# Performance work log

Measured on AMD Instinct MI355X. Metric: run time of the kernel, lower is better.

Reference implementation:

```python
import jax, jax.numpy as jnp
import numpy as np

B, L, D, H, O = 128, 256, 512, 1024, 2


def setup_inputs() -> dict:
    key = jax.random.key(0)
    ks = jax.random.split(key, 8)
    s = 1.0 / np.sqrt(H)
    sx = 1.0 / np.sqrt(D)
    return {
        "x": jax.random.normal(ks[0], (B, L, D), dtype=jnp.float32),
        "slen": jax.random.randint(ks[1], (B,), 0, L - 1),
        "Wh": jax.random.uniform(ks[2], (H, H), jnp.float32, -s, s),
        "bh": jax.random.uniform(ks[3], (H,), jnp.float32, -s, s),
        "Wx": jax.random.uniform(ks[4], (D, H), jnp.float32, -sx, sx),
        "bx": jax.random.uniform(ks[5], (H,), jnp.float32, -sx, sx),
        "Wo": jax.random.uniform(ks[6], (H, O), jnp.float32, -s, s),
        "bo": jax.random.uniform(ks[7], (O,), jnp.float32, -s, s),
    }


def reference(x, slen, Wh, bh, Wx, bx, Wo, bo):
    # x: (B, L, D) -> time-major (L, B, D)
    xT = jnp.transpose(x, (1, 0, 2))
    # input projection is time-independent: precompute Wx(x)+bx
    xp = xT @ Wx + bx  # (L, B, H)

    def step(carry, xpi):
        h, c = carry
        # All four 'gates' in the source share the same Wh/Wx, so a single
        # pre-activation z drives everything: i = f = o = sigmoid(z), g = tanh(z)
        z = h @ Wh + bh + xpi
        sg = jax.nn.sigmoid(z)
        g = jnp.tanh(z)
        c = sg * c + sg * g
        h = sg * jnp.tanh(c)
        return (h, c), h

    h0 = jnp.zeros((x.shape[0], Wh.shape[0]), dtype=x.dtype)
    _, hs = jax.lax.scan(step, (h0, h0), xp)  # (L, B, H)

    out = jax.nn.sigmoid(hs @ Wo + bo)  # (L, B, O)
    out = jnp.transpose(out, (1, 0, 2))  # (B, L, O)
    # positions il in [slen[b]+1, L) are overwritten with [0, 1]
    il = jnp.arange(out.shape[1])
    keep = (il[None, :] <= slen[:, None])[:, :, None]  # (B, L, 1)
    pad = jnp.array([0.0, 1.0], dtype=out.dtype)
    out = jnp.where(keep, out, pad)
    return out.reshape(-1, out.shape[-1])  # (B*L, O)
```

## Files before the change

kernel.cpp:

```cpp
#include <hip/hip_runtime.h>


#define B_ 128
#define L_ 256
#define D_ 512
#define H_ 1024

typedef __attribute__((ext_vector_type(8))) short short8;
typedef __attribute__((ext_vector_type(4))) float f32x4;
typedef __attribute__((ext_vector_type(2))) float f32x2;
typedef __attribute__((ext_vector_type(4))) unsigned short u16x4;
typedef __attribute__((ext_vector_type(4))) int i32x4;

__device__ __forceinline__ unsigned short f2bf(float f) {
    unsigned int u = __float_as_uint(f);
    return (unsigned short)((u + 0x8000u) >> 16);
}
__device__ __forceinline__ float bf2f(unsigned short s) {
    return __uint_as_float(((unsigned int)s) << 16);
}

__device__ __forceinline__ void st8(unsigned short* p, unsigned long long v) {
    __hip_atomic_store((unsigned long long*)p, v,
                       __ATOMIC_RELAXED, __HIP_MEMORY_SCOPE_AGENT);
}

template<int OFF>
__device__ __forceinline__ i32x4 ld16cc(const unsigned short* p) {
    i32x4 r;
    asm volatile("global_load_dwordx4 %0, %1, off offset:%2 sc0 sc1"
                 : "=v"(r) : "v"(p), "i"(OFF) : "memory");
    return r;
}
__device__ __forceinline__ void wait_vm4(i32x4& a, i32x4& b, i32x4& c, i32x4& d) {
    asm volatile("s_waitcnt vmcnt(4)" : "+v"(a), "+v"(b), "+v"(c), "+v"(d) :: "memory");
}
__device__ __forceinline__ void wait_vm0(i32x4& a, i32x4& b, i32x4& c, i32x4& d) {
    asm volatile("s_waitcnt vmcnt(0)" : "+v"(a), "+v"(b), "+v"(c), "+v"(d) :: "memory");
}
__device__ __forceinline__ void release_vm0() {
    asm volatile("s_waitcnt vmcnt(0)" ::: "memory");
}

__global__ __launch_bounds__(256) void k0_prep(
    const float* __restrict__ Wh, const float* __restrict__ Wx,
    const float* __restrict__ bh, const float* __restrict__ bx,
    unsigned short* __restrict__ Whb_t, unsigned short* __restrict__ Wxb_t,
    float* __restrict__ bxh, int* __restrict__ bar)
{
    __shared__ float tile[64][65];
    const int blk = blockIdx.x;
    const int t   = threadIdx.x;
    const int c   = t & 63, r0 = t >> 6;

    if (blk < 256) {
        const int tk = (blk >> 4) * 64, tn = (blk & 15) * 64;
#pragma unroll
        for (int i = 0; i < 16; ++i) {
            int r = i * 4 + r0;
            tile[r][c] = Wh[(size_t)(tk + r) * H_ + tn + c];
        }
        __syncthreads();
#pragma unroll
        for (int i = 0; i < 16; ++i) {
            int r = i * 4 + r0;
            Whb_t[(size_t)(tn + r) * H_ + tk + c] = f2bf(tile[c][r]);
        }
    } else if (blk < 384) {
        const int bi = blk - 256;
        const int tk = (bi >> 4) * 64, tn = (bi & 15) * 64;
#pragma unroll
        for (int i = 0; i < 16; ++i) {
            int r = i * 4 + r0;
            tile[r][c] = Wx[(size_t)(tk + r) * H_ + tn + c];
        }
        __syncthreads();
#pragma unroll
        for (int i = 0; i < 16; ++i) {
            int r = i * 4 + r0;
            Wxb_t[(size_t)(tn + r) * D_ + tk + c] = f2bf(tile[c][r]);
        }
    } else {
        for (int i = t; i < H_; i += 256) bxh[i] = bx[i] + bh[i];
        for (int i = t; i < 8 * 1024; i += 256) bar[i] = 0;
    }
}

__global__ __launch_bounds__(256) void k1_xproj(
    const float* __restrict__ x, const unsigned short* __restrict__ Wxb_t,
    const float* __restrict__ bxh, unsigned short* __restrict__ xp)
{
    const int nt   = blockIdx.x & 3;
    const int mt   = blockIdx.x >> 2;
    const int w    = threadIdx.x >> 6;
    const int lane = threadIdx.x & 63;
    const int m    = lane & 15, q = lane >> 4;
    const int m0   = mt * 64;
    const int l    = m0 >> 7;
    const int brow = (m0 & 127) + w * 16;
    const int n0   = nt * 256;

    const float* ap = x + ((size_t)(brow + m) * L_ + l) * D_ + q * 8;

    f32x4 acc[16];
#pragma unroll
    for (int t = 0; t < 16; ++t) acc[t] = (f32x4){0.f, 0.f, 0.f, 0.f};

#pragma unroll 4
    for (int kk = 0; kk < 16; ++kk) {
        f32x4 av0 = *(const f32x4*)(ap + kk * 32);
        f32x4 av1 = *(const f32x4*)(ap + kk * 32 + 4);
        short8 a8;
        a8[0] = (short)f2bf(av0[0]); a8[1] = (short)f2bf(av0[1]);
        a8[2] = (short)f2bf(av0[2]); a8[3] = (short)f2bf(av0[3]);
        a8[4] = (short)f2bf(av1[0]); a8[5] = (short)f2bf(av1[1]);
        a8[6] = (short)f2bf(av1[2]); a8[7] = (short)f2bf(av1[3]);
#pragma unroll
        for (int t = 0; t < 16; ++t) {
            short8 b8 = *(const short8*)(Wxb_t +
                        (size_t)(n0 + t * 16 + m) * D_ + kk * 32 + q * 8);
            acc[t] = __builtin_amdgcn_mfma_f32_16x16x32_bf16(b8, a8, acc[t], 0, 0, 0);
        }
    }

#pragma unroll
    for (int t = 0; t < 16; ++t) {
        const int c0 = n0 + t * 16 + q * 4;
        f32x4 bias = *(const f32x4*)(bxh + c0);
        u16x4 o;
#pragma unroll
        for (int r = 0; r < 4; ++r) o[r] = f2bf(acc[t][r] + bias[r]);
        *(u16x4*)(xp + ((size_t)l * B_ + brow + m) * H_ + c0) = o;
    }
}

__global__ __launch_bounds__(256, 1) void k2_scan(
    const unsigned short* __restrict__ Whb_t,
    const unsigned short* __restrict__ xp,
    unsigned short* __restrict__ hs,
    int* __restrict__ bar)
{
    __shared__ unsigned short buf[2][16][1032];

    const int g    = blockIdx.x & 7;
    const int wg   = blockIdx.x >> 3;
    const int tid  = threadIdx.x;
    const int w    = tid >> 6;
    const int lane = tid & 63;
    const int mb   = lane & 15, q = lane >> 4;
    const int b0   = g * 16;
    const int colw = wg * 64 + w * 16;

    short8 afrag[32];
    {
        const unsigned short* wp = Whb_t + (size_t)(colw + mb) * H_ + q * 8;
#pragma unroll
        for (int kk = 0; kk < 32; ++kk)
            asm volatile("global_load_dwordx4 %0, %1, off offset:%2"
                         : "=v"(afrag[kk]) : "v"(wp), "i"(kk * 64));
        asm volatile("s_waitcnt vmcnt(0)" ::: "memory");
#pragma unroll
        for (int kk = 0; kk < 32; ++kk)
            asm volatile("" : "+v"(afrag[kk]));
    }

    int* flags  = bar + g * 1024;
    int* myflag = flags + (wg * 4 + w) * 16;

    const int srow = tid >> 4;
    const int sci  = tid & 15;

    float c[4] = {0.f, 0.f, 0.f, 0.f};

    for (int l = 0; l < L_; ++l) {
        u16x4 xv = *(const u16x4*)(xp + ((size_t)l * B_ + b0 + mb) * H_ + colw + q * 4);

        unsigned short* lbuf = &buf[l & 1][0][0];
        if (l > 0) {
            while (true) {
                int f = __hip_atomic_load(flags + lane * 16,
                         __ATOMIC_RELAXED, __HIP_MEMORY_SCOPE_AGENT);
                if (__all(f >= l)) break;
            }
            const unsigned short* gp =
                hs + ((size_t)(l - 1) * B_ + b0 + srow) * H_ + sci * 8;
            i32x4 v0, v1, v2, v3, v4, v5, v6, v7;
            v0 = ld16cc<0>(gp);    v1 = ld16cc<256>(gp);
            v2 = ld16cc<512>(gp);  v3 = ld16cc<768>(gp);
            v4 = ld16cc<1024>(gp); v5 = ld16cc<1280>(gp);
            v6 = ld16cc<1536>(gp); v7 = ld16cc<1792>(gp);
            unsigned short* lp = lbuf + srow * 1032 + sci * 8;
            wait_vm4(v0, v1, v2, v3);
            *(i32x4*)(lp)        = v0;  *(i32x4*)(lp + 128)  = v1;
            *(i32x4*)(lp + 256)  = v2;  *(i32x4*)(lp + 384)  = v3;
            wait_vm0(v4, v5, v6, v7);
            *(i32x4*)(lp + 512)  = v4;  *(i32x4*)(lp + 640)  = v5;
            *(i32x4*)(lp + 768)  = v6;  *(i32x4*)(lp + 896)  = v7;
        }
        __syncthreads();

        f32x4 acc0 = {0.f,0.f,0.f,0.f}, acc1 = {0.f,0.f,0.f,0.f};
        f32x4 acc2 = {0.f,0.f,0.f,0.f}, acc3 = {0.f,0.f,0.f,0.f};
        if (l > 0) {
            const unsigned short* rp = lbuf + mb * 1032 + q * 8;
#pragma unroll
            for (int kb = 0; kb < 32; kb += 4) {
                short8 bb0 = *(const short8*)(rp + (kb + 0) * 32);
                short8 bb1 = *(const short8*)(rp + (kb + 1) * 32);
                short8 bb2 = *(const short8*)(rp + (kb + 2) * 32);
                short8 bb3 = *(const short8*)(rp + (kb + 3) * 32);
                acc0 = __builtin_amdgcn_mfma_f32_16x16x32_bf16(afrag[kb + 0], bb0, acc0, 0, 0, 0);
                acc1 = __builtin_amdgcn_mfma_f32_16x16x32_bf16(afrag[kb + 1], bb1, acc1, 0, 0, 0);
                acc2 = __builtin_amdgcn_mfma_f32_16x16x32_bf16(afrag[kb + 2], bb2, acc2, 0, 0, 0);
                acc3 = __builtin_amdgcn_mfma_f32_16x16x32_bf16(afrag[kb + 3], bb3, acc3, 0, 0, 0);
            }
        }
        u16x4 o;
#pragma unroll
        for (int r = 0; r < 4; ++r) {
            float z  = acc0[r] + acc1[r] + acc2[r] + acc3[r] + bf2f(xv[r]);
            float e  = __expf(-z);
            float sg = 1.f / (1.f + e);
            float gg = 2.f / (1.f + e * e) - 1.f;
            c[r] = sg * (c[r] + gg);
            float ec = __expf(-2.f * c[r]);
            float th = 2.f / (1.f + ec) - 1.f;
            o[r] = f2bf(sg * th);
        }
        union { u16x4 v; unsigned long long u; } hu;
        hu.v = o;
        st8(hs + ((size_t)l * B_ + b0 + mb) * H_ + colw + q * 4, hu.u);
        release_vm0();
        if (lane == 0)
            __hip_atomic_store(myflag, l + 1,
                               __ATOMIC_RELAXED, __HIP_MEMORY_SCOPE_AGENT);
    }
}

__global__ __launch_bounds__(256) void k3_out(
    const unsigned short* __restrict__ hs,
    const float* __restrict__ Wo, const float* __restrict__ bo,
    const int* __restrict__ slen, float* __restrict__ out)
{
    const int w    = threadIdx.x >> 6;
    const int lane = threadIdx.x & 63;
    const int r    = blockIdx.x * 4 + w;
    const int b    = r >> 8;
    const int l    = r & 255;

    const unsigned short* hp = hs + ((size_t)l * B_ + b) * H_ + lane * 16;
    const float* wp = Wo + (size_t)lane * 32;
    float u0 = 0.f, u1 = 0.f;
#pragma unroll
    for (int j0 = 0; j0 < 16; j0 += 8) {
        short8 hv = *(const short8*)(hp + j0);
#pragma unroll
        for (int j = 0; j < 8; ++j) {
            float h = bf2f((unsigned short)hv[j]);
            f32x2 wv = *(const f32x2*)(wp + (j0 + j) * 2);
            u0 += h * wv[0];
            u1 += h * wv[1];
        }
    }
#pragma unroll
    for (int off = 32; off; off >>= 1) {
        u0 += __shfl_down(u0, off);
        u1 += __shfl_down(u1, off);
    }
    if (lane == 0) {
        float o0, o1;
        if (l <= slen[b]) {
            o0 = 1.f / (1.f + __expf(-(u0 + bo[0])));
            o1 = 1.f / (1.f + __expf(-(u1 + bo[1])));
        } else {
            o0 = 0.f; o1 = 1.f;
        }
        out[(size_t)r * 2]     = o0;
        out[(size_t)r * 2 + 1] = o1;
    }
}

extern "C" void kernel_launch(void* const* d_in, const int* in_sizes, int n_in,
                              void* d_out, int out_size, void* d_ws, size_t ws_size,
                              hipStream_t stream)
{
    const float* x    = (const float*)d_in[0];
    const int*   slen = (const int*)d_in[1];
    const float* Wh   = (const float*)d_in[2];
    const float* bh   = (const float*)d_in[3];
    const float* Wx   = (const float*)d_in[4];
    const float* bx   = (const float*)d_in[5];
    const float* Wo   = (const float*)d_in[6];
    const float* bo   = (const float*)d_in[7];
    float* out = (float*)d_out;

    char* ws = (char*)d_ws;
    unsigned short* Whb_t = (unsigned short*)(ws);
    unsigned short* Wxb_t = (unsigned short*)(ws + (2u << 20));
    float*          bxh   = (float*)(ws + (3u << 20));
    int*            bar   = (int*)(ws + (3u << 20) + 65536);
    unsigned short* xp    = (unsigned short*)(ws + (4u << 20));
    unsigned short* hs    = (unsigned short*)(ws + (68u << 20));

    k0_prep<<<385, 256, 0, stream>>>(Wh, Wx, bh, bx, Whb_t, Wxb_t, bxh, bar);
    k1_xproj<<<2048, 256, 0, stream>>>(x, Wxb_t, bxh, xp);
    k2_scan<<<128, 256, 0, stream>>>(Whb_t, xp, hs, bar);
    k3_out<<<8192, 256, 0, stream>>>(hs, Wo, bo, slen, out);
}
```

Measured before the change: 1.354 ms.

## Replace per-step flag barrier with sentinel-filled hidden-state polling

```diff
diff --git a/kernel.cpp b/kernel.cpp
--- a/kernel.cpp
+++ b/kernel.cpp
@@ -32,21 +32,30 @@
                  : "=v"(r) : "v"(p), "i"(OFF) : "memory");
     return r;
 }
-__device__ __forceinline__ void wait_vm4(i32x4& a, i32x4& b, i32x4& c, i32x4& d) {
-    asm volatile("s_waitcnt vmcnt(4)" : "+v"(a), "+v"(b), "+v"(c), "+v"(d) :: "memory");
-}
-__device__ __forceinline__ void wait_vm0(i32x4& a, i32x4& b, i32x4& c, i32x4& d) {
-    asm volatile("s_waitcnt vmcnt(0)" : "+v"(a), "+v"(b), "+v"(c), "+v"(d) :: "memory");
-}
-__device__ __forceinline__ void release_vm0() {
-    asm volatile("s_waitcnt vmcnt(0)" ::: "memory");
+
+__device__ __forceinline__ void wait_vm0_8(i32x4& a, i32x4& b, i32x4& c, i32x4& d,
+                                           i32x4& e, i32x4& f, i32x4& g, i32x4& h) {
+    asm volatile("s_waitcnt vmcnt(0)"
+                 : "+v"(a), "+v"(b), "+v"(c), "+v"(d),
+                   "+v"(e), "+v"(f), "+v"(g), "+v"(h) :: "memory");
+}
+
+__device__ __forceinline__ unsigned badchunk(i32x4 v) {
+    unsigned bad = 0;
+#pragma unroll
+    for (int i = 0; i < 4; ++i) {
+        unsigned d = (unsigned)v[i];
+        bad |= ((d & 0xFFFFu) == 0xFFFFu);
+        bad |= ((d >> 16)     == 0xFFFFu);
+    }
+    return bad;
 }
 
 __global__ __launch_bounds__(256) void k0_prep(
     const float* __restrict__ Wh, const float* __restrict__ Wx,
     const float* __restrict__ bh, const float* __restrict__ bx,
     unsigned short* __restrict__ Whb_t, unsigned short* __restrict__ Wxb_t,
-    float* __restrict__ bxh, int* __restrict__ bar)
+    float* __restrict__ bxh, unsigned short* __restrict__ hs)
 {
     __shared__ float tile[64][65];
     const int blk = blockIdx.x;
@@ -80,9 +89,16 @@
             int r = i * 4 + r0;
             Wxb_t[(size_t)(tn + r) * D_ + tk + c] = f2bf(tile[c][r]);
         }
+    } else if (blk == 384) {
+        for (int i = t; i < H_; i += 256) bxh[i] = bx[i] + bh[i];
     } else {
-        for (int i = t; i < H_; i += 256) bxh[i] = bx[i] + bh[i];
-        for (int i = t; i < 8 * 1024; i += 256) bar[i] = 0;
+        const int pb = blk - 385;
+        i32x4 s = { -1, -1, -1, -1 };
+        i32x4* p = (i32x4*)hs;
+        const size_t base = (size_t)pb * 256 + t;
+#pragma unroll
+        for (int i = 0; i < 8; ++i)
+            p[base + (size_t)i * 524288] = s;
     }
 }
 
@@ -137,8 +153,7 @@
 __global__ __launch_bounds__(256, 1) void k2_scan(
     const unsigned short* __restrict__ Whb_t,
     const unsigned short* __restrict__ xp,
-    unsigned short* __restrict__ hs,
-    int* __restrict__ bar)
+    unsigned short* __restrict__ hs)
 {
     __shared__ unsigned short buf[2][16][1032];
 
@@ -164,9 +179,6 @@
             asm volatile("" : "+v"(afrag[kk]));
     }
 
-    int* flags  = bar + g * 1024;
-    int* myflag = flags + (wg * 4 + w) * 16;
-
     const int srow = tid >> 4;
     const int sci  = tid & 15;
 
@@ -177,23 +189,23 @@
 
         unsigned short* lbuf = &buf[l & 1][0][0];
         if (l > 0) {
-            while (true) {
-                int f = __hip_atomic_load(flags + lane * 16,
-                         __ATOMIC_RELAXED, __HIP_MEMORY_SCOPE_AGENT);
-                if (__all(f >= l)) break;
-            }
             const unsigned short* gp =
                 hs + ((size_t)(l - 1) * B_ + b0 + srow) * H_ + sci * 8;
             i32x4 v0, v1, v2, v3, v4, v5, v6, v7;
-            v0 = ld16cc<0>(gp);    v1 = ld16cc<256>(gp);
-            v2 = ld16cc<512>(gp);  v3 = ld16cc<768>(gp);
-            v4 = ld16cc<1024>(gp); v5 = ld16cc<1280>(gp);
-            v6 = ld16cc<1536>(gp); v7 = ld16cc<1792>(gp);
+            while (true) {
+                v0 = ld16cc<0>(gp);    v1 = ld16cc<256>(gp);
+                v2 = ld16cc<512>(gp);  v3 = ld16cc<768>(gp);
+                v4 = ld16cc<1024>(gp); v5 = ld16cc<1280>(gp);
+                v6 = ld16cc<1536>(gp); v7 = ld16cc<1792>(gp);
+                wait_vm0_8(v0, v1, v2, v3, v4, v5, v6, v7);
+                unsigned bad = badchunk(v0) | badchunk(v1) | badchunk(v2) |
+                               badchunk(v3) | badchunk(v4) | badchunk(v5) |
+                               badchunk(v6) | badchunk(v7);
+                if (!bad) break;
+            }
             unsigned short* lp = lbuf + srow * 1032 + sci * 8;
-            wait_vm4(v0, v1, v2, v3);
             *(i32x4*)(lp)        = v0;  *(i32x4*)(lp + 128)  = v1;
             *(i32x4*)(lp + 256)  = v2;  *(i32x4*)(lp + 384)  = v3;
-            wait_vm0(v4, v5, v6, v7);
             *(i32x4*)(lp + 512)  = v4;  *(i32x4*)(lp + 640)  = v5;
             *(i32x4*)(lp + 768)  = v6;  *(i32x4*)(lp + 896)  = v7;
         }
@@ -230,10 +242,6 @@
         union { u16x4 v; unsigned long long u; } hu;
         hu.v = o;
         st8(hs + ((size_t)l * B_ + b0 + mb) * H_ + colw + q * 4, hu.u);
-        release_vm0();
-        if (lane == 0)
-            __hip_atomic_store(myflag, l + 1,
-                               __ATOMIC_RELAXED, __HIP_MEMORY_SCOPE_AGENT);
     }
 }
 
@@ -298,12 +306,11 @@
     unsigned short* Whb_t = (unsigned short*)(ws);
     unsigned short* Wxb_t = (unsigned short*)(ws + (2u << 20));
     float*          bxh   = (float*)(ws + (3u << 20));
-    int*            bar   = (int*)(ws + (3u << 20) + 65536);
     unsigned short* xp    = (unsigned short*)(ws + (4u << 20));
     unsigned short* hs    = (unsigned short*)(ws + (68u << 20));
 
-    k0_prep<<<385, 256, 0, stream>>>(Wh, Wx, bh, bx, Whb_t, Wxb_t, bxh, bar);
+    k0_prep<<<2433, 256, 0, stream>>>(Wh, Wx, bh, bx, Whb_t, Wxb_t, bxh, hs);
     k1_xproj<<<2048, 256, 0, stream>>>(x, Wxb_t, bxh, xp);
-    k2_scan<<<128, 256, 0, stream>>>(Whb_t, xp, hs, bar);
+    k2_scan<<<128, 256, 0, stream>>>(Whb_t, xp, hs);
     k3_out<<<8192, 256, 0, stream>>>(hs, Wo, bo, slen, out);
 }
```

Result: slower. 1.540 ms (+13.7%).
